# Kernel tuning notes

Measured on AMD Instinct MI355X. Metric: run time of the kernel, lower is better.

The kernel has to match this reference:

```python
import jax, jax.numpy as jnp
import numpy as np

N = 50000      # nodes
E = 800000     # directed edges (before self loops)
F_IN = 2613    # raw feature dim (nn.Linear(2613, 256))
D = 256        # hidden dim, heads = 1
BN_EPS = 1e-5
NEG_SLOPE = 0.2  # PyG GATConv default negative_slope


def setup_inputs() -> dict:
    key = jax.random.key(0)
    ks = jax.random.split(key, 12)

    def glorot(k, shape):
        s = (6.0 / (shape[0] + shape[-1])) ** 0.5
        return jax.random.uniform(k, shape, jnp.float32, -s, s)

    zeros = lambda: jnp.zeros((D,), jnp.float32)
    ones = lambda: jnp.ones((D,), jnp.float32)
    return {
        "x": jax.random.normal(ks[0], (N, F_IN), dtype=jnp.float32),
        "edges": jax.random.randint(ks[1], (2, E), 0, N, dtype=jnp.int32),
        "W1": glorot(ks[2], (F_IN, D)), "b1": zeros(),
        "W2": glorot(ks[3], (D, D)), "b2": zeros(),
        "W3": glorot(ks[4], (D, D)), "b3": zeros(),
        "g1": ones(), "be1": zeros(),
        "g2": ones(), "be2": zeros(),
        "g3": ones(), "be3": zeros(),
        "Wg1": glorot(ks[5], (D, D)),
        "att_src1": glorot(ks[6], (D,)), "att_dst1": glorot(ks[7], (D,)),
        "bg1": zeros(), "g4": ones(), "be4": zeros(),
        "Wg2": glorot(ks[8], (D, D)),
        "att_src2": glorot(ks[9], (D,)), "att_dst2": glorot(ks[10], (D,)),
        "bg2": zeros(), "g5": ones(), "be5": zeros(),
    }


def batch_norm(h, gamma, beta):
    # BatchNorm1d in training mode: batch statistics over the node axis
    mu = h.mean(axis=0)
    var = h.var(axis=0)
    return (h - mu) * jax.lax.rsqrt(var + BN_EPS) * gamma + beta


def gat_conv(h, W, att_src, att_dst, bias, src, dst):
    # PyG GATConv, heads=1: shared linear for src/dst, additive attention,
    # leaky_relu scores, softmax over incoming edges per destination node.
    xl = h @ W                              # [N, D]
    a_src = xl @ att_src                    # [N]
    a_dst = xl @ att_dst                    # [N]
    e = jax.nn.leaky_relu(a_src[src] + a_dst[dst], NEG_SLOPE)  # [E+N]
    m = jax.ops.segment_max(jax.lax.stop_gradient(e), dst, num_segments=N)
    w = jnp.exp(e - m[dst])
    denom = jax.ops.segment_sum(w, dst, num_segments=N)
    alpha = w / (denom[dst] + 1e-16)        # [E+N]
    out = jax.ops.segment_sum(alpha[:, None] * xl[src], dst, num_segments=N)
    return out + bias


def reference(x, edges, W1, b1, W2, b2, W3, b3, g1, be1, g2, be2, g3, be3,
              Wg1, att_src1, att_dst1, bg1, g4, be4,
              Wg2, att_src2, att_dst2, bg2, g5, be5):
    # PyG GATConv default add_self_loops=True
    loops = jnp.arange(N, dtype=edges.dtype)
    src = jnp.concatenate([edges[0], loops])
    dst = jnp.concatenate([edges[1], loops])

    h = jax.nn.elu(batch_norm(x @ W1 + b1, g1, be1))
    h = jax.nn.elu(batch_norm(h @ W2 + b2, g2, be2))
    h = jax.nn.elu(batch_norm(h @ W3 + b3, g3, be3))
    h = gat_conv(h, Wg1, att_src1, att_dst1, bg1, src, dst)
    h = jax.nn.elu(batch_norm(h, g4, be4))
    h = gat_conv(h, Wg2, att_src2, att_dst2, bg2, src, dst)
    h = jax.nn.elu(batch_norm(h, g5, be5))
    return h
```

## Files before the change

### kernel.cpp

```cpp
#include <hip/hip_runtime.h>

#define DEV __device__ __forceinline__

typedef __attribute__((ext_vector_type(4))) float f32x4;
typedef __attribute__((ext_vector_type(8))) short short8;

DEV float bf2f(unsigned short u) {
    union { unsigned int i; float f; } c;
    c.i = ((unsigned int)u) << 16;
    return c.f;
}
DEV unsigned short f2bf(float f) {
    union { float f; unsigned int i; } c;
    c.f = f;
    unsigned int u = c.i;
    u += 0x7FFFu + ((u >> 16) & 1u);
    return (unsigned short)(u >> 16);
}

__global__ void cvt_pad_k(const float* __restrict__ x, unsigned short* __restrict__ xb,
                          int M, int K, int Kp) {
    const int gpr = Kp >> 3;
    const long long total = (long long)M * gpr;
    for (long long g = blockIdx.x * (long long)blockDim.x + threadIdx.x; g < total;
         g += (long long)gridDim.x * blockDim.x) {
        const int row = (int)(g / gpr);
        const int c8  = (int)(g - (long long)row * gpr);
        const int k0  = c8 * 8;
        const float* src = x + (size_t)row * K + k0;
        unsigned int w[4];
        if (k0 + 8 <= K) {
            f32x4 v0 = *(const f32x4*)(src);
            f32x4 v1 = *(const f32x4*)(src + 4);
            w[0] = (unsigned int)f2bf(v0[0]) | ((unsigned int)f2bf(v0[1]) << 16);
            w[1] = (unsigned int)f2bf(v0[2]) | ((unsigned int)f2bf(v0[3]) << 16);
            w[2] = (unsigned int)f2bf(v1[0]) | ((unsigned int)f2bf(v1[1]) << 16);
            w[3] = (unsigned int)f2bf(v1[2]) | ((unsigned int)f2bf(v1[3]) << 16);
        } else {
            unsigned short o[8];
            #pragma unroll
            for (int j = 0; j < 8; ++j) o[j] = (k0 + j < K) ? f2bf(src[j]) : (unsigned short)0;
            w[0] = o[0] | ((unsigned int)o[1] << 16);
            w[1] = o[2] | ((unsigned int)o[3] << 16);
            w[2] = o[4] | ((unsigned int)o[5] << 16);
            w[3] = o[6] | ((unsigned int)o[7] << 16);
        }
        *(uint4*)(xb + (size_t)row * Kp + k0) = *(uint4*)w;
    }
}

template<bool STATS>
__launch_bounds__(512)
__global__ void gemm_k(const unsigned short* __restrict__ A,
                       const unsigned short* __restrict__ Bt,
                       unsigned short* __restrict__ C,
                       float* __restrict__ st,
                       int M, int lda, int ldb, int ksteps)
{
    __shared__ __align__(16) unsigned short As[3][128 * 64];
    __shared__ __align__(16) unsigned short Bs[3][256 * 64];
    const int t    = threadIdx.x;
    const int wid  = t >> 6;
    const int lane = t & 63;
    const int wr   = wid >> 2;
    const int wc   = wid & 3;
    const int m0   = blockIdx.x * 128;

    f32x4 acc[4][4] = {};

    auto stage = [&](int buf, int ks) {
        const int k0 = ks * 64;
        #pragma unroll
        for (int is = 0; is < 2; ++is) {
            const int rbase = wid * 16 + is * 8;
            const int rr  = rbase + (lane >> 3);
            const int csw = (lane & 7) ^ (rr & 7);
            __builtin_amdgcn_global_load_lds(
                (const __attribute__((address_space(1))) void*)(A + (size_t)(m0 + rr) * lda + k0 + csw * 8),
                (__attribute__((address_space(3))) void*)(&As[buf][rbase * 64]),
                16, 0, 0);
        }
        #pragma unroll
        for (int is = 0; is < 4; ++is) {
            const int rbase = wid * 32 + is * 8;
            const int rr  = rbase + (lane >> 3);
            const int csw = (lane & 7) ^ (rr & 7);
            __builtin_amdgcn_global_load_lds(
                (const __attribute__((address_space(1))) void*)(Bt + (size_t)rr * ldb + k0 + csw * 8),
                (__attribute__((address_space(3))) void*)(&Bs[buf][rbase * 64]),
                16, 0, 0);
        }
    };
    auto compute = [&](int buf) {
        #pragma unroll
        for (int kk = 0; kk < 2; ++kk) {
            short8 af[4], bfr[4];
            #pragma unroll
            for (int mi = 0; mi < 4; ++mi) {
                const int r   = wr * 64 + mi * 16 + (lane & 15);
                const int csw = (kk * 4 + (lane >> 4)) ^ (r & 7);
                af[mi] = *(const short8*)(&As[buf][r * 64 + csw * 8]);
            }
            #pragma unroll
            for (int ni = 0; ni < 4; ++ni) {
                const int r   = wc * 64 + ni * 16 + (lane & 15);
                const int csw = (kk * 4 + (lane >> 4)) ^ (r & 7);
                bfr[ni] = *(const short8*)(&Bs[buf][r * 64 + csw * 8]);
            }
            #pragma unroll
            for (int mi = 0; mi < 4; ++mi)
                #pragma unroll
                for (int ni = 0; ni < 4; ++ni)
                    acc[mi][ni] = __builtin_amdgcn_mfma_f32_16x16x32_bf16(
                        af[mi], bfr[ni], acc[mi][ni], 0, 0, 0);
        }
    };

    stage(0, 0);
    __builtin_amdgcn_sched_barrier(0);
    stage(1, 1);
    __builtin_amdgcn_sched_barrier(0);
    stage(2, 2);
    asm volatile("s_waitcnt vmcnt(12)" ::: "memory");
    __builtin_amdgcn_sched_barrier(0);
    __builtin_amdgcn_s_barrier();
    __builtin_amdgcn_sched_barrier(0);

    int cur = 0;
    for (int k = 0; k < ksteps; ++k) {
        compute(cur);
        if (k + 1 >= ksteps) break;
        __builtin_amdgcn_sched_barrier(0);
        __builtin_amdgcn_s_barrier();
        __builtin_amdgcn_sched_barrier(0);
        if (k + 3 < ksteps) {
            stage(cur, k + 3);
            asm volatile("s_waitcnt vmcnt(12)" ::: "memory");
        } else if (k + 2 < ksteps) {
            asm volatile("s_waitcnt vmcnt(6)" ::: "memory");
        } else {
            asm volatile("s_waitcnt vmcnt(0)" ::: "memory");
        }
        __builtin_amdgcn_sched_barrier(0);
        __builtin_amdgcn_s_barrier();
        __builtin_amdgcn_sched_barrier(0);
        cur = (cur == 2) ? 0 : cur + 1;
    }

    #pragma unroll
    for (int mi = 0; mi < 4; ++mi) {
        #pragma unroll
        for (int ni = 0; ni < 4; ++ni) {
            const int col = wc * 64 + ni * 16 + (lane & 15);
            #pragma unroll
            for (int rg = 0; rg < 4; ++rg) {
                const int m = m0 + wr * 64 + mi * 16 + (lane >> 4) * 4 + rg;
                if (m < M)
                    C[(size_t)m * 256 + col] = f2bf(acc[mi][ni][rg]);
            }
        }
    }
    if constexpr (STATS) {
        #pragma unroll
        for (int ni = 0; ni < 4; ++ni) {
            float s = 0.f, q = 0.f;
            #pragma unroll
            for (int mi = 0; mi < 4; ++mi)
                #pragma unroll
                for (int rg = 0; rg < 4; ++rg) {
                    const int m = m0 + wr * 64 + mi * 16 + (lane >> 4) * 4 + rg;
                    const float v = (m < M) ? acc[mi][ni][rg] : 0.f;
                    s += v; q += v * v;
                }
            s += __shfl_xor(s, 16); q += __shfl_xor(q, 16);
            s += __shfl_xor(s, 32); q += __shfl_xor(q, 32);
            if (lane < 16) {
                const int col = wc * 64 + ni * 16 + lane;
                atomicAdd(&st[col], s);
                atomicAdd(&st[256 + col], q);
            }
        }
    }
}

__global__ void wtrans_k(const float* __restrict__ W, unsigned short* __restrict__ WT,
                         int K, int ldb) {
    int total = 256 * ldb;
    for (int idx = blockIdx.x * blockDim.x + threadIdx.x; idx < total;
         idx += gridDim.x * blockDim.x) {
        int n = idx / ldb, k = idx - n * ldb;
        WT[idx] = f2bf(k < K ? W[(size_t)k * 256 + n] : 0.f);
    }
}

__global__ void colstats_k(const unsigned short* __restrict__ h, float* st, int total4) {
    const int gid    = blockIdx.x * 256 + threadIdx.x;
    const int stride = gridDim.x * 256;
    float4 s = {0.f, 0.f, 0.f, 0.f}, q = {0.f, 0.f, 0.f, 0.f};
    for (int i = gid; i < total4; i += stride) {
        ushort4 v = ((const ushort4*)h)[i];
        float x0 = bf2f(v.x), x1 = bf2f(v.y), x2 = bf2f(v.z), x3 = bf2f(v.w);
        s.x += x0; s.y += x1; s.z += x2; s.w += x3;
        q.x += x0 * x0; q.y += x1 * x1; q.z += x2 * x2; q.w += x3 * x3;
    }
    __shared__ float red[2][4][64][4];
    const int wid = threadIdx.x >> 6, lane = threadIdx.x & 63;
    *(float4*)&red[0][wid][lane][0] = s;
    *(float4*)&red[1][wid][lane][0] = q;
    __syncthreads();
    if (wid == 0) {
        float4 s0 = *(float4*)&red[0][0][lane][0];
        float4 q0 = *(float4*)&red[1][0][lane][0];
        #pragma unroll
        for (int w = 1; w < 4; ++w) {
            float4 sw = *(float4*)&red[0][w][lane][0];
            float4 qw = *(float4*)&red[1][w][lane][0];
            s0.x += sw.x; s0.y += sw.y; s0.z += sw.z; s0.w += sw.w;
            q0.x += qw.x; q0.y += qw.y; q0.z += qw.z; q0.w += qw.w;
        }
        atomicAdd(&st[lane * 4 + 0], s0.x);
        atomicAdd(&st[lane * 4 + 1], s0.y);
        atomicAdd(&st[lane * 4 + 2], s0.z);
        atomicAdd(&st[lane * 4 + 3], s0.w);
        atomicAdd(&st[256 + lane * 4 + 0], q0.x);
        atomicAdd(&st[256 + lane * 4 + 1], q0.y);
        atomicAdd(&st[256 + lane * 4 + 2], q0.z);
        atomicAdd(&st[256 + lane * 4 + 3], q0.w);
    }
}

template<bool OUT_F32>
__global__ void bnelu_k(const unsigned short* __restrict__ h,
                        const float* __restrict__ st, const float* __restrict__ g,
                        const float* __restrict__ be, void* __restrict__ outp,
                        int total4, float invN) {
    const int gid    = blockIdx.x * 256 + threadIdx.x;
    const int stride = gridDim.x * 256;
    const int c      = (gid << 2) & 255;
    float sc[4], sh[4];
    #pragma unroll
    for (int j = 0; j < 4; ++j) {
        float mu  = st[c + j] * invN;
        float var = st[256 + c + j] * invN - mu * mu;
        float s   = g[c + j] * rsqrtf(var + 1e-5f);
        sc[j] = s;
        sh[j] = be[c + j] - mu * s;
    }
    for (int i = gid; i < total4; i += stride) {
        ushort4 v = ((const ushort4*)h)[i];
        float y0 = fmaf(bf2f(v.x), sc[0], sh[0]);
        float y1 = fmaf(bf2f(v.y), sc[1], sh[1]);
        float y2 = fmaf(bf2f(v.z), sc[2], sh[2]);
        float y3 = fmaf(bf2f(v.w), sc[3], sh[3]);
        y0 = y0 > 0.f ? y0 : expm1f(y0);
        y1 = y1 > 0.f ? y1 : expm1f(y1);
        y2 = y2 > 0.f ? y2 : expm1f(y2);
        y3 = y3 > 0.f ? y3 : expm1f(y3);
        if (OUT_F32) {
            float4 o; o.x = y0; o.y = y1; o.z = y2; o.w = y3;
            ((float4*)outp)[i] = o;
        } else {
            ushort4 o;
            o.x = f2bf(y0); o.y = f2bf(y1); o.z = f2bf(y2); o.w = f2bf(y3);
            ((ushort4*)outp)[i] = o;
        }
    }
}

__global__ void adot_k(const unsigned short* __restrict__ xl, const float* __restrict__ as_,
                       const float* __restrict__ ad_, float* __restrict__ a_src,
                       float* __restrict__ a_dst, int N) {
    int w = (blockIdx.x * blockDim.x + threadIdx.x) >> 6;
    int lane = threadIdx.x & 63;
    if (w >= N) return;
    ushort4 v = *(const ushort4*)(xl + (size_t)w * 256 + lane * 4);
    float4 s4 = *(const float4*)(as_ + lane * 4);
    float4 d4 = *(const float4*)(ad_ + lane * 4);
    float x0 = bf2f(v.x), x1 = bf2f(v.y), x2 = bf2f(v.z), x3 = bf2f(v.w);
    float ps = x0 * s4.x + x1 * s4.y + x2 * s4.z + x3 * s4.w;
    float pd = x0 * d4.x + x1 * d4.y + x2 * d4.z + x3 * d4.w;
    #pragma unroll
    for (int off = 32; off; off >>= 1) {
        ps += __shfl_xor(ps, off);
        pd += __shfl_xor(pd, off);
    }
    if (lane == 0) { a_src[w] = ps; a_dst[w] = pd; }
}

DEV float lrelu(float e) { return e > 0.f ? e : 0.2f * e; }

__global__ void gat_k(const unsigned short* __restrict__ xl, const float* __restrict__ a_src,
                      const float* __restrict__ a_dst, const int* __restrict__ csr,
                      const int* __restrict__ indptr, unsigned short* __restrict__ out, int N) {
    int d = (blockIdx.x * blockDim.x + threadIdx.x) >> 6;
    int lane = threadIdx.x & 63;
    if (d >= N) return;
    int beg = indptr[d], end = indptr[d + 1];
    float adst = a_dst[d];

    float m = -1e30f, s = 0.f;
    for (int i = beg + lane; i < end; i += 64) {
        float e  = lrelu(a_src[csr[i]] + adst);
        float nm = fmaxf(m, e);
        s = s * __expf(m - nm) + __expf(e - nm);
        m = nm;
    }
    float mx = m;
    #pragma unroll
    for (int off = 32; off; off >>= 1) mx = fmaxf(mx, __shfl_xor(mx, off));
    s *= __expf(m - mx);
    #pragma unroll
    for (int off = 32; off; off >>= 1) s += __shfl_xor(s, off);
    float inv = 1.f / (s + 1e-16f);

    float4 A0 = {0,0,0,0}, A1 = {0,0,0,0}, A2 = {0,0,0,0}, A3 = {0,0,0,0};
    int i = beg;
    for (; i + 4 <= end; i += 4) {
        int s0 = csr[i], s1 = csr[i+1], s2 = csr[i+2], s3 = csr[i+3];
        float w0 = __expf(lrelu(a_src[s0] + adst) - mx) * inv;
        float w1 = __expf(lrelu(a_src[s1] + adst) - mx) * inv;
        float w2 = __expf(lrelu(a_src[s2] + adst) - mx) * inv;
        float w3 = __expf(lrelu(a_src[s3] + adst) - mx) * inv;
        ushort4 v0 = *(const ushort4*)(xl + (size_t)s0 * 256 + lane * 4);
        ushort4 v1 = *(const ushort4*)(xl + (size_t)s1 * 256 + lane * 4);
        ushort4 v2 = *(const ushort4*)(xl + (size_t)s2 * 256 + lane * 4);
        ushort4 v3 = *(const ushort4*)(xl + (size_t)s3 * 256 + lane * 4);
        A0.x += w0 * bf2f(v0.x); A0.y += w0 * bf2f(v0.y); A0.z += w0 * bf2f(v0.z); A0.w += w0 * bf2f(v0.w);
        A1.x += w1 * bf2f(v1.x); A1.y += w1 * bf2f(v1.y); A1.z += w1 * bf2f(v1.z); A1.w += w1 * bf2f(v1.w);
        A2.x += w2 * bf2f(v2.x); A2.y += w2 * bf2f(v2.y); A2.z += w2 * bf2f(v2.z); A2.w += w2 * bf2f(v2.w);
        A3.x += w3 * bf2f(v3.x); A3.y += w3 * bf2f(v3.y); A3.z += w3 * bf2f(v3.z); A3.w += w3 * bf2f(v3.w);
    }
    for (; i < end; ++i) {
        int sidx = csr[i];
        float w = __expf(lrelu(a_src[sidx] + adst) - mx) * inv;
        ushort4 v = *(const ushort4*)(xl + (size_t)sidx * 256 + lane * 4);
        A0.x += w * bf2f(v.x); A0.y += w * bf2f(v.y);
        A0.z += w * bf2f(v.z); A0.w += w * bf2f(v.w);
    }
    ushort4 o;
    o.x = f2bf(A0.x + A1.x + A2.x + A3.x);
    o.y = f2bf(A0.y + A1.y + A2.y + A3.y);
    o.z = f2bf(A0.z + A1.z + A2.z + A3.z);
    o.w = f2bf(A0.w + A1.w + A2.w + A3.w);
    *(ushort4*)(out + (size_t)d * 256 + lane * 4) = o;
}

__global__ void hist_k(const int* __restrict__ edges, int* deg, int E, int N) {
    int total = E + N;
    for (int i = blockIdx.x * blockDim.x + threadIdx.x; i < total;
         i += gridDim.x * blockDim.x) {
        int dd = (i < E) ? edges[E + i] : (i - E);
        atomicAdd(&deg[dd], 1);
    }
}

__global__ void scan1_k(const int* __restrict__ deg, int* iscan, int* bsum, int N) {
    int i = blockIdx.x * 256 + threadIdx.x;
    int lane = threadIdx.x & 63, wid = threadIdx.x >> 6;
    int v = (i < N) ? deg[i] : 0;
    #pragma unroll
    for (int off = 1; off < 64; off <<= 1) {
        int u = __shfl_up(v, off);
        if (lane >= off) v += u;
    }
    __shared__ int wsum[4];
    if (lane == 63) wsum[wid] = v;
    __syncthreads();
    #pragma unroll
    for (int w = 0; w < 3; ++w) if (wid > w) v += wsum[w];
    if (i < N) iscan[i] = v;
    if (threadIdx.x == 255) bsum[blockIdx.x] = v;
}

__global__ void scan2_k(int* bsum, int nb) {
    int t = threadIdx.x;
    int lane = t & 63, wid = t >> 6;
    int v = (t < nb) ? bsum[t] : 0;
    int orig = v;
    #pragma unroll
    for (int off = 1; off < 64; off <<= 1) {
        int u = __shfl_up(v, off);
        if (lane >= off) v += u;
    }
    __shared__ int wsum[4];
    if (lane == 63) wsum[wid] = v;
    __syncthreads();
    #pragma unroll
    for (int w = 0; w < 3; ++w) if (wid > w) v += wsum[w];
    if (t < nb) bsum[t] = v - orig;
}

__global__ void scan3_k(const int* __restrict__ iscan, const int* __restrict__ boff,
                        int* indptr, int N) {
    int i = blockIdx.x * 256 + threadIdx.x;
    if (i < N) indptr[i + 1] = iscan[i] + boff[blockIdx.x];
    if (i == 0) indptr[0] = 0;
}

__global__ void copy_k(const int* __restrict__ a, int* b, int N) {
    for (int i = blockIdx.x * blockDim.x + threadIdx.x; i < N;
         i += gridDim.x * blockDim.x) b[i] = a[i];
}

__global__ void scatter_k(const int* __restrict__ edges, int* pos, int* csr, int E, int N) {
    int total = E + N;
    for (int i = blockIdx.x * blockDim.x + threadIdx.x; i < total;
         i += gridDim.x * blockDim.x) {
        int s  = (i < E) ? edges[i]     : (i - E);
        int dd = (i < E) ? edges[E + i] : (i - E);
        int slot = atomicAdd(&pos[dd], 1);
        csr[slot] = s;
    }
}

extern "C" void kernel_launch(void* const* d_in, const int* in_sizes, int n_in,
                              void* d_out, int out_size, void* d_ws, size_t ws_size,
                              hipStream_t stream) {
    const float* x     = (const float*)d_in[0];
    const int*   edges = (const int*)d_in[1];
    const float* W1 = (const float*)d_in[2];
    const float* W2 = (const float*)d_in[4];
    const float* W3 = (const float*)d_in[6];
    const float* g1 = (const float*)d_in[8],  *be1 = (const float*)d_in[9];
    const float* g2 = (const float*)d_in[10], *be2 = (const float*)d_in[11];
    const float* g3 = (const float*)d_in[12], *be3 = (const float*)d_in[13];
    const float* Wg1 = (const float*)d_in[14];
    const float* as1 = (const float*)d_in[15], *ad1 = (const float*)d_in[16];
    const float* g4 = (const float*)d_in[18], *be4 = (const float*)d_in[19];
    const float* Wg2 = (const float*)d_in[20];
    const float* as2 = (const float*)d_in[21], *ad2 = (const float*)d_in[22];
    const float* g5 = (const float*)d_in[24], *be5 = (const float*)d_in[25];

    const int N    = out_size / 256;
    const int K1   = in_sizes[0] / N;
    const int E    = in_sizes[1] / 2;
    const int Etot = E + N;
    const int ks1  = (K1 + 63) / 64;
    const int ldb1 = ks1 * 64;

    char* p = (char*)d_ws;
    auto alloc = [&](size_t bytes) {
        char* r = p;
        p += (bytes + 255) & ~(size_t)255;
        return r;
    };
    unsigned short* W1T  = (unsigned short*)alloc((size_t)256 * ldb1 * 2);
    unsigned short* W2T  = (unsigned short*)alloc(256 * 256 * 2);
    unsigned short* W3T  = (unsigned short*)alloc(256 * 256 * 2);
    unsigned short* Wg1T = (unsigned short*)alloc(256 * 256 * 2);
    unsigned short* Wg2T = (unsigned short*)alloc(256 * 256 * 2);
    unsigned short* xb   = (unsigned short*)alloc((size_t)N * ldb1 * 2);
    unsigned short* ha   = (unsigned short*)alloc((size_t)N * 256 * 2);
    unsigned short* hb   = (unsigned short*)alloc((size_t)N * 256 * 2);
    unsigned short* xl   = (unsigned short*)alloc((size_t)N * 256 * 2);
    float* a_src  = (float*)alloc((size_t)N * 4);
    float* a_dst  = (float*)alloc((size_t)N * 4);
    int*   deg    = (int*)alloc((size_t)N * 4);
    int*   iscan  = (int*)alloc((size_t)N * 4);
    int*   bsum   = (int*)alloc(1024);
    int*   indptr = (int*)alloc((size_t)(N + 1) * 4);
    int*   pos    = (int*)alloc((size_t)N * 4);
    int*   csr    = (int*)alloc((size_t)Etot * 4);
    float* st     = (float*)alloc(512 * 4);
    (void)alloc(1 << 19);
    float* out = (float*)d_out;

    const int nb = (N + 255) / 256;
    const int eg = (Etot + 255) / 256;
    const int gb = (N + 127) / 128;
    const int t4 = N * 64;
    const float invN = 1.f / (float)N;

    hipMemsetAsync(deg, 0, (size_t)N * 4, stream);
    hist_k<<<eg, 256, 0, stream>>>(edges, deg, E, N);
    scan1_k<<<nb, 256, 0, stream>>>(deg, iscan, bsum, N);
    scan2_k<<<1, 256, 0, stream>>>(bsum, nb);
    scan3_k<<<nb, 256, 0, stream>>>(iscan, bsum, indptr, N);
    copy_k<<<nb, 256, 0, stream>>>(indptr, pos, N);
    scatter_k<<<eg, 256, 0, stream>>>(edges, pos, csr, E, N);

    wtrans_k<<<(256 * ldb1 + 255) / 256, 256, 0, stream>>>(W1, W1T, K1, ldb1);
    wtrans_k<<<256, 256, 0, stream>>>(W2, W2T, 256, 256);
    wtrans_k<<<256, 256, 0, stream>>>(W3, W3T, 256, 256);
    wtrans_k<<<256, 256, 0, stream>>>(Wg1, Wg1T, 256, 256);
    wtrans_k<<<256, 256, 0, stream>>>(Wg2, Wg2T, 256, 256);
    cvt_pad_k<<<2048, 256, 0, stream>>>(x, xb, N, K1, ldb1);

    hipMemsetAsync(st, 0, 2048, stream);
    gemm_k<true><<<gb, 512, 0, stream>>>(xb, W1T, ha, st, N, ldb1, ldb1, ks1);
    bnelu_k<false><<<2048, 256, 0, stream>>>(ha, st, g1, be1, ha, t4, invN);

    hipMemsetAsync(st, 0, 2048, stream);
    gemm_k<true><<<gb, 512, 0, stream>>>(ha, W2T, hb, st, N, 256, 256, 4);
    bnelu_k<false><<<2048, 256, 0, stream>>>(hb, st, g2, be2, hb, t4, invN);

    hipMemsetAsync(st, 0, 2048, stream);
    gemm_k<true><<<gb, 512, 0, stream>>>(hb, W3T, ha, st, N, 256, 256, 4);
    bnelu_k<false><<<2048, 256, 0, stream>>>(ha, st, g3, be3, ha, t4, invN);

    gemm_k<false><<<gb, 512, 0, stream>>>(ha, Wg1T, xl, st, N, 256, 256, 4);
    adot_k<<<(N + 3) / 4, 256, 0, stream>>>(xl, as1, ad1, a_src, a_dst, N);
    gat_k<<<(N + 3) / 4, 256, 0, stream>>>(xl, a_src, a_dst, csr, indptr, hb, N);
    hipMemsetAsync(st, 0, 2048, stream);
    colstats_k<<<1024, 256, 0, stream>>>(hb, st, t4);
    bnelu_k<false><<<2048, 256, 0, stream>>>(hb, st, g4, be4, hb, t4, invN);

    gemm_k<false><<<gb, 512, 0, stream>>>(hb, Wg2T, xl, st, N, 256, 256, 4);
    adot_k<<<(N + 3) / 4, 256, 0, stream>>>(xl, as2, ad2, a_src, a_dst, N);
    gat_k<<<(N + 3) / 4, 256, 0, stream>>>(xl, a_src, a_dst, csr, indptr, ha, N);
    hipMemsetAsync(st, 0, 2048, stream);
    colstats_k<<<1024, 256, 0, stream>>>(ha, st, t4);
    bnelu_k<true><<<2048, 256, 0, stream>>>(ha, st, g5, be5, out, t4, invN);
}
```

Measured before the change: 966.4 us.

## Fuse prep kernels, attention dots into GEMM epilogue, consolidate memsets

Merges the x conversion and all five weight transposes into one prep kernel, and folds the scan copy into the scan finalize. The attention dot products move into the GAT GEMM epilogue, using per-row shuffle reductions and atomics. The many stats memsets become one memset over a contiguous zeroed region with separate stats slots per layer, and MFMA sections get raised wave priority. This cuts kernel launches and a full re-read of xl per GAT layer, at the cost of extra atomics and epilogue register pressure. The epilogue uses fp32 accumulators rather than the bf16-rounded xl, so attention logits may differ slightly.

```diff
diff --git a/kernel.cpp b/kernel.cpp
--- a/kernel.cpp
+++ b/kernel.cpp
@@ -18,43 +18,70 @@
     return (unsigned short)(u >> 16);
 }
 
-__global__ void cvt_pad_k(const float* __restrict__ x, unsigned short* __restrict__ xb,
-                          int M, int K, int Kp) {
-    const int gpr = Kp >> 3;
-    const long long total = (long long)M * gpr;
-    for (long long g = blockIdx.x * (long long)blockDim.x + threadIdx.x; g < total;
-         g += (long long)gridDim.x * blockDim.x) {
-        const int row = (int)(g / gpr);
-        const int c8  = (int)(g - (long long)row * gpr);
-        const int k0  = c8 * 8;
-        const float* src = x + (size_t)row * K + k0;
-        unsigned int w[4];
-        if (k0 + 8 <= K) {
-            f32x4 v0 = *(const f32x4*)(src);
-            f32x4 v1 = *(const f32x4*)(src + 4);
-            w[0] = (unsigned int)f2bf(v0[0]) | ((unsigned int)f2bf(v0[1]) << 16);
-            w[1] = (unsigned int)f2bf(v0[2]) | ((unsigned int)f2bf(v0[3]) << 16);
-            w[2] = (unsigned int)f2bf(v1[0]) | ((unsigned int)f2bf(v1[1]) << 16);
-            w[3] = (unsigned int)f2bf(v1[2]) | ((unsigned int)f2bf(v1[3]) << 16);
-        } else {
-            unsigned short o[8];
-            #pragma unroll
-            for (int j = 0; j < 8; ++j) o[j] = (k0 + j < K) ? f2bf(src[j]) : (unsigned short)0;
-            w[0] = o[0] | ((unsigned int)o[1] << 16);
-            w[1] = o[2] | ((unsigned int)o[3] << 16);
-            w[2] = o[4] | ((unsigned int)o[5] << 16);
-            w[3] = o[6] | ((unsigned int)o[7] << 16);
-        }
-        *(uint4*)(xb + (size_t)row * Kp + k0) = *(uint4*)w;
-    }
-}
-
-template<bool STATS>
+#define XB_B 2048
+__global__ void prep_k(const float* __restrict__ x,
+                       const float* __restrict__ W1, const float* __restrict__ W2,
+                       const float* __restrict__ W3, const float* __restrict__ Wg1,
+                       const float* __restrict__ Wg2,
+                       unsigned short* __restrict__ xb,
+                       unsigned short* __restrict__ WTbase,
+                       int M, int K1, int ldb1) {
+    if (blockIdx.x < XB_B) {
+        const int gpr = ldb1 >> 3;
+        const long long total = (long long)M * gpr;
+        for (long long g = blockIdx.x * (long long)blockDim.x + threadIdx.x; g < total;
+             g += (long long)XB_B * blockDim.x) {
+            const int row = (int)(g / gpr);
+            const int c8  = (int)(g - (long long)row * gpr);
+            const int k0  = c8 * 8;
+            const float* src = x + (size_t)row * K1 + k0;
+            unsigned int w[4];
+            if (k0 + 8 <= K1) {
+                f32x4 v0 = *(const f32x4*)(src);
+                f32x4 v1 = *(const f32x4*)(src + 4);
+                w[0] = (unsigned int)f2bf(v0[0]) | ((unsigned int)f2bf(v0[1]) << 16);
+                w[1] = (unsigned int)f2bf(v0[2]) | ((unsigned int)f2bf(v0[3]) << 16);
+                w[2] = (unsigned int)f2bf(v1[0]) | ((unsigned int)f2bf(v1[1]) << 16);
+                w[3] = (unsigned int)f2bf(v1[2]) | ((unsigned int)f2bf(v1[3]) << 16);
+            } else {
+                unsigned short o[8];
+                #pragma unroll
+                for (int j = 0; j < 8; ++j) o[j] = (k0 + j < K1) ? f2bf(src[j]) : (unsigned short)0;
+                w[0] = o[0] | ((unsigned int)o[1] << 16);
+                w[1] = o[2] | ((unsigned int)o[3] << 16);
+                w[2] = o[4] | ((unsigned int)o[5] << 16);
+                w[3] = o[6] | ((unsigned int)o[7] << 16);
+            }
+            *(uint4*)(xb + (size_t)row * ldb1 + k0) = *(uint4*)w;
+        }
+    } else {
+        const int w1n   = 256 * ldb1;
+        const int total = w1n + 4 * 65536;
+        const int wblk  = gridDim.x - XB_B;
+        for (int idx = (blockIdx.x - XB_B) * blockDim.x + threadIdx.x; idx < total;
+             idx += wblk * blockDim.x) {
+            const float* W; int K, ldb, i;
+            if (idx < w1n) { W = W1; K = K1; ldb = ldb1; i = idx; }
+            else {
+                int r = (idx - w1n) >> 16;
+                i = (idx - w1n) & 65535;
+                W = (r == 0) ? W2 : (r == 1) ? W3 : (r == 2) ? Wg1 : Wg2;
+                K = 256; ldb = 256;
+            }
+            int n = i / ldb, k = i - n * ldb;
+            WTbase[idx] = f2bf(k < K ? W[(size_t)k * 256 + n] : 0.f);
+        }
+    }
+}
+
+template<bool STATS, bool ADOT>
 __launch_bounds__(512)
 __global__ void gemm_k(const unsigned short* __restrict__ A,
                        const unsigned short* __restrict__ Bt,
                        unsigned short* __restrict__ C,
                        float* __restrict__ st,
+                       const float* __restrict__ avs, const float* __restrict__ avd,
+                       float* __restrict__ a_src, float* __restrict__ a_dst,
                        int M, int lda, int ldb, int ksteps)
 {
     __shared__ __align__(16) unsigned short As[3][128 * 64];
@@ -107,12 +134,14 @@
                 const int csw = (kk * 4 + (lane >> 4)) ^ (r & 7);
                 bfr[ni] = *(const short8*)(&Bs[buf][r * 64 + csw * 8]);
             }
+            __builtin_amdgcn_s_setprio(1);
             #pragma unroll
             for (int mi = 0; mi < 4; ++mi)
                 #pragma unroll
                 for (int ni = 0; ni < 4; ++ni)
                     acc[mi][ni] = __builtin_amdgcn_mfma_f32_16x16x32_bf16(
                         af[mi], bfr[ni], acc[mi][ni], 0, 0, 0);
+            __builtin_amdgcn_s_setprio(0);
         }
     };
 
@@ -181,15 +210,35 @@
             }
         }
     }
-}
-
-__global__ void wtrans_k(const float* __restrict__ W, unsigned short* __restrict__ WT,
-                         int K, int ldb) {
-    int total = 256 * ldb;
-    for (int idx = blockIdx.x * blockDim.x + threadIdx.x; idx < total;
-         idx += gridDim.x * blockDim.x) {
-        int n = idx / ldb, k = idx - n * ldb;
-        WT[idx] = f2bf(k < K ? W[(size_t)k * 256 + n] : 0.f);
+    if constexpr (ADOT) {
+        #pragma unroll
+        for (int mi = 0; mi < 4; ++mi) {
+            float ps[4] = {0.f, 0.f, 0.f, 0.f};
+            float pd[4] = {0.f, 0.f, 0.f, 0.f};
+            #pragma unroll
+            for (int ni = 0; ni < 4; ++ni) {
+                const int col = wc * 64 + ni * 16 + (lane & 15);
+                const float a_s = avs[col], a_d = avd[col];
+                #pragma unroll
+                for (int rg = 0; rg < 4; ++rg) {
+                    ps[rg] += acc[mi][ni][rg] * a_s;
+                    pd[rg] += acc[mi][ni][rg] * a_d;
+                }
+            }
+            #pragma unroll
+            for (int rg = 0; rg < 4; ++rg) {
+                #pragma unroll
+                for (int off = 1; off < 16; off <<= 1) {
+                    ps[rg] += __shfl_xor(ps[rg], off);
+                    pd[rg] += __shfl_xor(pd[rg], off);
+                }
+                const int m = m0 + wr * 64 + mi * 16 + (lane >> 4) * 4 + rg;
+                if ((lane & 15) == 0 && m < M) {
+                    atomicAdd(&a_src[m], ps[rg]);
+                    atomicAdd(&a_dst[m], pd[rg]);
+                }
+            }
+        }
     }
 }
 
@@ -267,26 +316,6 @@
     }
 }
 
-__global__ void adot_k(const unsigned short* __restrict__ xl, const float* __restrict__ as_,
-                       const float* __restrict__ ad_, float* __restrict__ a_src,
-                       float* __restrict__ a_dst, int N) {
-    int w = (blockIdx.x * blockDim.x + threadIdx.x) >> 6;
-    int lane = threadIdx.x & 63;
-    if (w >= N) return;
-    ushort4 v = *(const ushort4*)(xl + (size_t)w * 256 + lane * 4);
-    float4 s4 = *(const float4*)(as_ + lane * 4);
-    float4 d4 = *(const float4*)(ad_ + lane * 4);
-    float x0 = bf2f(v.x), x1 = bf2f(v.y), x2 = bf2f(v.z), x3 = bf2f(v.w);
-    float ps = x0 * s4.x + x1 * s4.y + x2 * s4.z + x3 * s4.w;
-    float pd = x0 * d4.x + x1 * d4.y + x2 * d4.z + x3 * d4.w;
-    #pragma unroll
-    for (int off = 32; off; off >>= 1) {
-        ps += __shfl_xor(ps, off);
-        pd += __shfl_xor(pd, off);
-    }
-    if (lane == 0) { a_src[w] = ps; a_dst[w] = pd; }
-}
-
 DEV float lrelu(float e) { return e > 0.f ? e : 0.2f * e; }
 
 __global__ void gat_k(const unsigned short* __restrict__ xl, const float* __restrict__ a_src,
@@ -390,16 +419,15 @@
     if (t < nb) bsum[t] = v - orig;
 }
 
-__global__ void scan3_k(const int* __restrict__ iscan, const int* __restrict__ boff,
-                        int* indptr, int N) {
+__global__ void scan3copy_k(const int* __restrict__ iscan, const int* __restrict__ boff,
+                            const int* __restrict__ deg, int* indptr, int* pos, int N) {
     int i = blockIdx.x * 256 + threadIdx.x;
-    if (i < N) indptr[i + 1] = iscan[i] + boff[blockIdx.x];
+    if (i < N) {
+        int v = iscan[i] + boff[blockIdx.x];
+        indptr[i + 1] = v;
+        pos[i] = v - deg[i];
+    }
     if (i == 0) indptr[0] = 0;
-}
-
-__global__ void copy_k(const int* __restrict__ a, int* b, int N) {
-    for (int i = blockIdx.x * blockDim.x + threadIdx.x; i < N;
-         i += gridDim.x * blockDim.x) b[i] = a[i];
 }
 
 __global__ void scatter_k(const int* __restrict__ edges, int* pos, int* csr, int E, int N) {
@@ -453,15 +481,19 @@
     unsigned short* ha   = (unsigned short*)alloc((size_t)N * 256 * 2);
     unsigned short* hb   = (unsigned short*)alloc((size_t)N * 256 * 2);
     unsigned short* xl   = (unsigned short*)alloc((size_t)N * 256 * 2);
-    float* a_src  = (float*)alloc((size_t)N * 4);
-    float* a_dst  = (float*)alloc((size_t)N * 4);
+    char* zero_base = p;
     int*   deg    = (int*)alloc((size_t)N * 4);
+    float* st     = (float*)alloc(5 * 512 * 4);
+    float* asrc1  = (float*)alloc((size_t)N * 4);
+    float* adst1  = (float*)alloc((size_t)N * 4);
+    float* asrc2  = (float*)alloc((size_t)N * 4);
+    float* adst2  = (float*)alloc((size_t)N * 4);
+    size_t zero_bytes = (size_t)(p - zero_base);
     int*   iscan  = (int*)alloc((size_t)N * 4);
     int*   bsum   = (int*)alloc(1024);
     int*   indptr = (int*)alloc((size_t)(N + 1) * 4);
     int*   pos    = (int*)alloc((size_t)N * 4);
     int*   csr    = (int*)alloc((size_t)Etot * 4);
-    float* st     = (float*)alloc(512 * 4);
     (void)alloc(1 << 19);
     float* out = (float*)d_out;
 
@@ -471,44 +503,38 @@
     const int t4 = N * 64;
     const float invN = 1.f / (float)N;
 
-    hipMemsetAsync(deg, 0, (size_t)N * 4, stream);
+    hipMemsetAsync(zero_base, 0, zero_bytes, stream);
+
     hist_k<<<eg, 256, 0, stream>>>(edges, deg, E, N);
     scan1_k<<<nb, 256, 0, stream>>>(deg, iscan, bsum, N);
     scan2_k<<<1, 256, 0, stream>>>(bsum, nb);
-    scan3_k<<<nb, 256, 0, stream>>>(iscan, bsum, indptr, N);
-    copy_k<<<nb, 256, 0, stream>>>(indptr, pos, N);
+    scan3copy_k<<<nb, 256, 0, stream>>>(iscan, bsum, deg, indptr, pos, N);
     scatter_k<<<eg, 256, 0, stream>>>(edges, pos, csr, E, N);
 
-    wtrans_k<<<(256 * ldb1 + 255) / 256, 256, 0, stream>>>(W1, W1T, K1, ldb1);
-    wtrans_k<<<256, 256, 0, stream>>>(W2, W2T, 256, 256);
-    wtrans_k<<<256, 256, 0, stream>>>(W3, W3T, 256, 256);
-    wtrans_k<<<256, 256, 0, stream>>>(Wg1, Wg1T, 256, 256);
-    wtrans_k<<<256, 256, 0, stream>>>(Wg2, Wg2T, 256, 256);
-    cvt_pad_k<<<2048, 256, 0, stream>>>(x, xb, N, K1, ldb1);
-
-    hipMemsetAsync(st, 0, 2048, stream);
-    gemm_k<true><<<gb, 512, 0, stream>>>(xb, W1T, ha, st, N, ldb1, ldb1, ks1);
+    prep_k<<<XB_B + 1600, 256, 0, stream>>>(x, W1, W2, W3, Wg1, Wg2,
+                                            xb, W1T, N, K1, ldb1);
+
+    gemm_k<true, false><<<gb, 512, 0, stream>>>(xb, W1T, ha, st, nullptr, nullptr,
+                                                nullptr, nullptr, N, ldb1, ldb1, ks1);
     bnelu_k<false><<<2048, 256, 0, stream>>>(ha, st, g1, be1, ha, t4, invN);
 
-    hipMemsetAsync(st, 0, 2048, stream);
-    gemm_k<true><<<gb, 512, 0, stream>>>(ha, W2T, hb, st, N, 256, 256, 4);
-    bnelu_k<false><<<2048, 256, 0, stream>>>(hb, st, g2, be2, hb, t4, invN);
-
-    hipMemsetAsync(st, 0, 2048, stream);
-    gemm_k<true><<<gb, 512, 0, stream>>>(hb, W3T, ha, st, N, 256, 256, 4);
-    bnelu_k<false><<<2048, 256, 0, stream>>>(ha, st, g3, be3, ha, t4, invN);
-
-    gemm_k<false><<<gb, 512, 0, stream>>>(ha, Wg1T, xl, st, N, 256, 256, 4);
-    adot_k<<<(N + 3) / 4, 256, 0, stream>>>(xl, as1, ad1, a_src, a_dst, N);
-    gat_k<<<(N + 3) / 4, 256, 0, stream>>>(xl, a_src, a_dst, csr, indptr, hb, N);
-    hipMemsetAsync(st, 0, 2048, stream);
-    colstats_k<<<1024, 256, 0, stream>>>(hb, st, t4);
-    bnelu_k<false><<<2048, 256, 0, stream>>>(hb, st, g4, be4, hb, t4, invN);
-
-    gemm_k<false><<<gb, 512, 0, stream>>>(hb, Wg2T, xl, st, N, 256, 256, 4);
-    adot_k<<<(N + 3) / 4, 256, 0, stream>>>(xl, as2, ad2, a_src, a_dst, N);
-    gat_k<<<(N + 3) / 4, 256, 0, stream>>>(xl, a_src, a_dst, csr, indptr, ha, N);
-    hipMemsetAsync(st, 0, 2048, stream);
-    colstats_k<<<1024, 256, 0, stream>>>(ha, st, t4);
-    bnelu_k<true><<<2048, 256, 0, stream>>>(ha, st, g5, be5, out, t4, invN);
-}
+    gemm_k<true, false><<<gb, 512, 0, stream>>>(ha, W2T, hb, st + 512, nullptr, nullptr,
+                                                nullptr, nullptr, N, 256, 256, 4);
+    bnelu_k<false><<<2048, 256, 0, stream>>>(hb, st + 512, g2, be2, hb, t4, invN);
+
+    gemm_k<true, false><<<gb, 512, 0, stream>>>(hb, W3T, ha, st + 1024, nullptr, nullptr,
+                                                nullptr, nullptr, N, 256, 256, 4);
+    bnelu_k<false><<<2048, 256, 0, stream>>>(ha, st + 1024, g3, be3, ha, t4, invN);
+
+    gemm_k<false, true><<<gb, 512, 0, stream>>>(ha, Wg1T, xl, nullptr, as1, ad1,
+                                                asrc1, adst1, N, 256, 256, 4);
+    gat_k<<<(N + 3) / 4, 256, 0, stream>>>(xl, asrc1, adst1, csr, indptr, hb, N);
+    colstats_k<<<1024, 256, 0, stream>>>(hb, st + 1536, t4);
+    bnelu_k<false><<<2048, 256, 0, stream>>>(hb, st + 1536, g4, be4, hb, t4, invN);
+
+    gemm_k<false, true><<<gb, 512, 0, stream>>>(hb, Wg2T, xl, nullptr, as2, ad2,
+                                                asrc2, adst2, N, 256, 256, 4);
+    gat_k<<<(N + 3) / 4, 256, 0, stream>>>(xl, asrc2, adst2, csr, indptr, ha, N);
+    colstats_k<<<1024, 256, 0, stream>>>(ha, st + 2048, t4);
+    bnelu_k<true><<<2048, 256, 0, stream>>>(ha, st + 2048, g5, be5, out, t4, invN);
+}
```

After: 940.9 us. 2.6% less time.
